# Performance work log

Hardware: AMD Instinct MI355X
Metric: run time of the kernel (lower is better)

## Reference

```python
import jax, jax.numpy as jnp
import numpy as np

ALPHA = 0.7
GAMMA = 2
EPS = 1e-07


def setup_inputs() -> dict:
    key = jax.random.key(0)
    k1, k2 = jax.random.split(key)
    shape = (64, 3, 288, 512)
    output = jax.random.uniform(k1, shape, dtype=jnp.float32)  # sigmoid probs in (0,1)
    targets = jax.random.randint(k2, shape, 0, 2, dtype=jnp.int32)  # binary heatmap
    return {"output": output, "targets": targets}


def reference(output, targets):
    p = output.reshape(-1)
    y = targets.reshape(-1)
    pos = y == 1
    # pt = p where y==1 else 1-p
    pt = jnp.where(pos, p, 1.0 - p)
    log = -jnp.log(pt)
    # original replaces inf (pt == 0) with 1e-7
    log = jnp.where(jnp.isinf(log), EPS, log)
    focal = (1.0 - pt) ** GAMMA * log
    # alpha weighting applied to positive-class elements
    focal = jnp.where(pos, focal * ALPHA, focal)
    return jnp.mean(focal)
```

## Files before the change

kernel.cpp:

```cpp
#include <hip/hip_runtime.h>
#include <math.h>

#define ALPHA 0.7f
#define EPSF  1e-7f

__device__ __forceinline__ float focal_elem(float p, int y) {
    const bool pos = (y == 1);
    const float pt = pos ? p : 1.0f - p;
    float lg = -__logf(pt);
    if (isinf(lg)) lg = EPSF;
    const float om = 1.0f - pt;
    float f = om * om * lg;
    return pos ? f * ALPHA : f;
}

template <int BLOCK>
__device__ __forceinline__ float block_reduce(float acc) {
    #pragma unroll
    for (int off = 32; off > 0; off >>= 1)
        acc += __shfl_down(acc, off, 64);
    __shared__ float smem[BLOCK / 64];
    const int lane = threadIdx.x & 63;
    const int wave = threadIdx.x >> 6;
    if (lane == 0) smem[wave] = acc;
    __syncthreads();
    float s = 0.0f;
    if (threadIdx.x == 0) {
        #pragma unroll
        for (int w = 0; w < BLOCK / 64; ++w) s += smem[w];
    }
    return s;
}

__device__ __forceinline__ float focal4(const float4 pv, const int4 yv) {
    float a = focal_elem(pv.x, yv.x);
    a += focal_elem(pv.y, yv.y);
    a += focal_elem(pv.z, yv.z);
    a += focal_elem(pv.w, yv.w);
    return a;
}

template <int BLOCK>
__global__ void __launch_bounds__(BLOCK)
focal_partial(const float* __restrict__ p, const int* __restrict__ y,
              float* __restrict__ partial, long long n) {
    const long long n4 = n >> 2;
    const float4* __restrict__ p4 = (const float4*)p;
    const int4*   __restrict__ y4 = (const int4*)y;
    const long long stride = (long long)gridDim.x * BLOCK;
    long long i = (long long)blockIdx.x * BLOCK + threadIdx.x;

    float acc = 0.0f;
    for (; i + stride < n4; i += 2 * stride) {
        const float4 pv0 = p4[i];
        const int4   yv0 = y4[i];
        const float4 pv1 = p4[i + stride];
        const int4   yv1 = y4[i + stride];
        acc += focal4(pv0, yv0);
        acc += focal4(pv1, yv1);
    }
    for (; i < n4; i += stride) {
        acc += focal4(p4[i], y4[i]);
    }
    const long long tail = n4 << 2;
    for (long long j = tail + (long long)blockIdx.x * BLOCK + threadIdx.x; j < n; j += stride)
        acc += focal_elem(p[j], y[j]);

    const float s = block_reduce<BLOCK>(acc);
    if (threadIdx.x == 0) partial[blockIdx.x] = s;
}

template <int BLOCK>
__global__ void __launch_bounds__(BLOCK)
focal_final(const float* __restrict__ partial, int nparts,
            float* __restrict__ out, long long n) {
    float acc = 0.0f;
    for (int i = threadIdx.x; i < nparts; i += BLOCK) acc += partial[i];
    const float s = block_reduce<BLOCK>(acc);
    if (threadIdx.x == 0) out[0] = s / (float)n;
}

extern "C" void kernel_launch(void* const* d_in, const int* in_sizes, int n_in,
                              void* d_out, int out_size, void* d_ws, size_t ws_size,
                              hipStream_t stream) {
    const float* p = (const float*)d_in[0];
    const int*   y = (const int*)d_in[1];
    float* out = (float*)d_out;
    float* partial = (float*)d_ws;

    const long long n = (long long)in_sizes[0];
    constexpr int BLOCK = 256;
    constexpr int NBLOCKS = 2048;

    focal_partial<BLOCK><<<NBLOCKS, BLOCK, 0, stream>>>(p, y, partial, n);
    focal_final<BLOCK><<<1, BLOCK, 0, stream>>>(partial, NBLOCKS, out, n);
}
```

Baseline: 238.7 us.

## Assign contiguous fully unrolled chunks per block instead of grid-stride loop

Replaces the fixed 2048-block grid-stride loop with one contiguous chunk of 4096 float4 per block. Each thread runs 16 fully unrolled iterations, so more loads can be in flight per thread. The grid size is now derived from the input size, the scalar tail moves to a single thread of the last block, and launch bounds request 4 blocks per CU. The cost is more register pressure from the unrolled loads and a grid that scales with n.

```diff
diff --git a/kernel.cpp b/kernel.cpp
--- a/kernel.cpp
+++ b/kernel.cpp
@@ -12,6 +12,14 @@
     const float om = 1.0f - pt;
     float f = om * om * lg;
     return pos ? f * ALPHA : f;
+}
+
+__device__ __forceinline__ float focal4(const float4 pv, const int4 yv) {
+    float a = focal_elem(pv.x, yv.x);
+    a += focal_elem(pv.y, yv.y);
+    a += focal_elem(pv.z, yv.z);
+    a += focal_elem(pv.w, yv.w);
+    return a;
 }
 
 template <int BLOCK>
@@ -32,42 +40,35 @@
     return s;
 }
 
-__device__ __forceinline__ float focal4(const float4 pv, const int4 yv) {
-    float a = focal_elem(pv.x, yv.x);
-    a += focal_elem(pv.y, yv.y);
-    a += focal_elem(pv.z, yv.z);
-    a += focal_elem(pv.w, yv.w);
-    return a;
-}
-
-template <int BLOCK>
-__global__ void __launch_bounds__(BLOCK)
+template <int BLOCK, int VPB>
+__global__ void __launch_bounds__(BLOCK, 4)
 focal_partial(const float* __restrict__ p, const int* __restrict__ y,
               float* __restrict__ partial, long long n) {
+    constexpr int ITERS = VPB / BLOCK;
     const long long n4 = n >> 2;
     const float4* __restrict__ p4 = (const float4*)p;
     const int4*   __restrict__ y4 = (const int4*)y;
-    const long long stride = (long long)gridDim.x * BLOCK;
-    long long i = (long long)blockIdx.x * BLOCK + threadIdx.x;
+    const long long base = (long long)blockIdx.x * VPB;
+    const int t = threadIdx.x;
 
     float acc = 0.0f;
-    for (; i + stride < n4; i += 2 * stride) {
-        const float4 pv0 = p4[i];
-        const int4   yv0 = y4[i];
-        const float4 pv1 = p4[i + stride];
-        const int4   yv1 = y4[i + stride];
-        acc += focal4(pv0, yv0);
-        acc += focal4(pv1, yv1);
+    if (base + VPB <= n4) {
+        #pragma unroll
+        for (int u = 0; u < ITERS; ++u) {
+            const long long i = base + (long long)u * BLOCK + t;
+            acc += focal4(p4[i], y4[i]);
+        }
+    } else {
+        for (long long i = base + t; i < n4; i += BLOCK)
+            acc += focal4(p4[i], y4[i]);
     }
-    for (; i < n4; i += stride) {
-        acc += focal4(p4[i], y4[i]);
+    if (blockIdx.x == gridDim.x - 1 && t == 0) {
+        for (long long j = n4 << 2; j < n; ++j)
+            acc += focal_elem(p[j], y[j]);
     }
-    const long long tail = n4 << 2;
-    for (long long j = tail + (long long)blockIdx.x * BLOCK + threadIdx.x; j < n; j += stride)
-        acc += focal_elem(p[j], y[j]);
 
     const float s = block_reduce<BLOCK>(acc);
-    if (threadIdx.x == 0) partial[blockIdx.x] = s;
+    if (t == 0) partial[blockIdx.x] = s;
 }
 
 template <int BLOCK>
@@ -90,8 +91,11 @@
 
     const long long n = (long long)in_sizes[0];
     constexpr int BLOCK = 256;
-    constexpr int NBLOCKS = 2048;
+    constexpr int VPB = 4096;
+    const long long n4 = n >> 2;
+    int nblocks = (int)((n4 + VPB - 1) / VPB);
+    if (nblocks < 1) nblocks = 1;
 
-    focal_partial<BLOCK><<<NBLOCKS, BLOCK, 0, stream>>>(p, y, partial, n);
-    focal_final<BLOCK><<<1, BLOCK, 0, stream>>>(partial, NBLOCKS, out, n);
+    focal_partial<BLOCK, VPB><<<nblocks, BLOCK, 0, stream>>>(p, y, partial, n);
+    focal_final<BLOCK><<<1, BLOCK, 0, stream>>>(partial, nblocks, out, n);
 }
```

Result: no change. 243.3 us (+2.0%).
